# Kernel optimization log

Measured on AMD Instinct MI355X. Metric: run time of the kernel, lower is better.

Reference implementation:

```python
import jax, jax.numpy as jnp
import numpy as np

B, C, H, W = 32, 128, 56, 56
CMAX, OUT, KS, K = 128, 256, 3, 4
HID = 64  # attn_fc hidden width


def setup_inputs() -> dict:
    key = jax.random.key(0)
    ks = jax.random.split(key, 6)
    x = jax.random.normal(ks[0], (B, C, H, W), dtype=jnp.float32)
    weight_bank = jax.random.normal(ks[1], (K, OUT, CMAX, KS, KS), dtype=jnp.float32)
    fc1_w = jax.random.normal(ks[2], (HID, CMAX), dtype=jnp.float32) * (1.0 / np.sqrt(CMAX))
    fc1_b = jnp.zeros((HID,), dtype=jnp.float32)
    fc2_w = jax.random.normal(ks[3], (K, HID), dtype=jnp.float32) * (1.0 / np.sqrt(HID))
    fc2_b = jnp.zeros((K,), dtype=jnp.float32)
    return {"x": x, "weight_bank": weight_bank, "fc1_w": fc1_w, "fc1_b": fc1_b,
            "fc2_w": fc2_w, "fc2_b": fc2_b}


def reference(x, weight_bank, fc1_w, fc1_b, fc2_w, fc2_b):
    b, c, h, w = x.shape
    # AdaptiveAvgPool2d(1) on zero-channel-padded input -> mean over HW, pad channel dim
    pooled = jnp.mean(x, axis=(2, 3))                       # [B, C]
    pooled = jnp.pad(pooled, ((0, 0), (0, CMAX - c)))       # [B, CMAX]
    hdn = jax.nn.relu(pooled @ fc1_w.T + fc1_b)             # [B, 64]
    attn = jax.nn.softmax(hdn @ fc2_w.T + fc2_b, axis=-1)   # [B, K]
    # per-sample kernel synthesis
    weight = jnp.einsum('bk,kocij->bocij', attn, weight_bank[:, :, :c])  # [B,O,C,k,k]
    # single grouped conv instead of B separate conv launches
    lhs = x.reshape(1, b * c, h, w)
    rhs = weight.reshape(b * OUT, c, KS, KS)
    p = KS // 2
    out = jax.lax.conv_general_dilated(
        lhs, rhs, window_strides=(1, 1), padding=[(p, p), (p, p)],
        feature_group_count=b,
        dimension_numbers=('NCHW', 'OIHW', 'NCHW'))
    return out.reshape(b, OUT, h, w)
```

## Files before the change

### kernel.cpp

```cpp
#include <hip/hip_runtime.h>
#include <hip/hip_bf16.h>

#define B_    32
#define C_    128
#define H_    56
#define W_    56
#define OUT_  256
#define K_    4
#define HID_  64
#define HW_   (H_*W_)
#define KV_   (C_*9)
#define PH_   58
#define PW_   58
#define PP_   (PH_*PW_)

typedef __attribute__((ext_vector_type(8))) short short8_t;
typedef __attribute__((ext_vector_type(4))) float float4_t;

typedef __hip_bfloat16 bf16;

__device__ __forceinline__ short f2bf(float v) {
    union { bf16 h; short s; } u; u.h = __float2bfloat16(v); return u.s;
}

typedef __attribute__((address_space(1))) const unsigned int* gas_t;
typedef __attribute__((address_space(3))) unsigned int* las_t;

__device__ __forceinline__ void gl_lds16(const short* g, short* l) {
    __builtin_amdgcn_global_load_lds((gas_t)(const void*)g, (las_t)(void*)l, 16, 0, 0);
}

__global__ __launch_bounds__(256) void dc_xt(const float* __restrict__ x,
                                             short* __restrict__ xTp,
                                             float* __restrict__ pooled) {
    int b = blockIdx.y, n0 = blockIdx.x * 128;
    __shared__ short t[C_][130];
    int lane = threadIdx.x & 63;
    for (int i = threadIdx.x; i < C_*128; i += 256) {
        int c = i >> 7, nn = i & 127;
        int pp = n0 + nn;
        int py = pp / PW_, px = pp - py*PW_;
        bool valid = (pp < PP_) & (py >= 1) & (py <= H_) & (px >= 1) & (px <= W_);
        float v = valid ? x[((size_t)b*C_ + c)*HW_ + (py-1)*W_ + (px-1)] : 0.f;
        t[c][nn] = f2bf(v);
        float s = v;
        for (int off = 32; off > 0; off >>= 1) s += __shfl_down(s, off, 64);
        if (lane == 0 && s != 0.f) atomicAdd(&pooled[b*C_ + c], s);
    }
    __syncthreads();
    for (int i = threadIdx.x; i < 64*128; i += 256) {
        int nn = i >> 6, c2 = (i & 63) * 2;
        int pp = n0 + nn;
        if (pp < PP_) {
            union { unsigned short u[2]; unsigned v; } pk;
            pk.u[0] = (unsigned short)t[c2][nn];
            pk.u[1] = (unsigned short)t[c2+1][nn];
            *(unsigned*)&xTp[((size_t)b*PP_ + pp)*C_ + c2] = pk.v;
        }
    }
}

__global__ __launch_bounds__(64) void dc_attn(const float* __restrict__ pooled,
                                              const float* __restrict__ fc1w,
                                              const float* __restrict__ fc1b,
                                              const float* __restrict__ fc2w,
                                              const float* __restrict__ fc2b,
                                              float* __restrict__ attn) {
    int b = blockIdx.x, h = threadIdx.x;
    __shared__ float pl[C_];
    __shared__ float hdn[HID_];
    __shared__ float logit[K_];
    pl[h]      = pooled[b*C_ + h]      * (1.0f / HW_);
    pl[h + 64] = pooled[b*C_ + 64 + h] * (1.0f / HW_);
    __syncthreads();
    float s = fc1b[h];
    #pragma unroll 8
    for (int c = 0; c < C_; ++c) s += pl[c] * fc1w[h*C_ + c];
    hdn[h] = fmaxf(s, 0.f);
    __syncthreads();
    if (h < K_) {
        float t = fc2b[h];
        #pragma unroll 8
        for (int j = 0; j < HID_; ++j) t += hdn[j] * fc2w[h*HID_ + j];
        logit[h] = t;
    }
    __syncthreads();
    if (h == 0) {
        float m = fmaxf(fmaxf(logit[0], logit[1]), fmaxf(logit[2], logit[3]));
        float e0 = __expf(logit[0]-m), e1 = __expf(logit[1]-m);
        float e2 = __expf(logit[2]-m), e3 = __expf(logit[3]-m);
        float inv = 1.0f / (e0+e1+e2+e3);
        attn[b*K_+0]=e0*inv; attn[b*K_+1]=e1*inv;
        attn[b*K_+2]=e2*inv; attn[b*K_+3]=e3*inv;
    }
}

__global__ __launch_bounds__(256) void dc_wsynth(const float* __restrict__ bank,
                                                 const float* __restrict__ attn,
                                                 bf16* __restrict__ Ws) {
    int o = blockIdx.x;
    int b0 = blockIdx.y * 8;
    __shared__ float wb[4*KV_];
    for (int i = threadIdx.x; i < 4*KV_; i += 256) {
        int kk = i / KV_, r = i - kk*KV_;
        wb[i] = bank[((size_t)kk*OUT_ + o)*KV_ + r];
    }
    __syncthreads();
    for (int bi = 0; bi < 8; ++bi) {
        int b = b0 + bi;
        float a0 = attn[b*K_+0], a1 = attn[b*K_+1];
        float a2 = attn[b*K_+2], a3 = attn[b*K_+3];
        unsigned* dst = (unsigned*)&Ws[((size_t)b*OUT_ + o)*KV_];
        for (int ii = threadIdx.x; ii < KV_/2; ii += 256) {
            int i0 = 2*ii;
            int tap0 = i0 >> 7, c0 = i0 & 127;
            int i1 = i0 + 1;
            int tap1 = i1 >> 7, c1 = i1 & 127;
            float v0 = a0*wb[c0*9+tap0] + a1*wb[KV_+c0*9+tap0]
                     + a2*wb[2*KV_+c0*9+tap0] + a3*wb[3*KV_+c0*9+tap0];
            float v1 = a0*wb[c1*9+tap1] + a1*wb[KV_+c1*9+tap1]
                     + a2*wb[2*KV_+c1*9+tap1] + a3*wb[3*KV_+c1*9+tap1];
            union { unsigned short u[2]; unsigned v; } pk;
            pk.u[0] = (unsigned short)f2bf(v0);
            pk.u[1] = (unsigned short)f2bf(v1);
            dst[ii] = pk.v;
        }
    }
}

__global__ __launch_bounds__(256) void dc_gemm(const short* __restrict__ Ws,
                                               const short* __restrict__ xTp,
                                               float* __restrict__ out) {
    const int b  = blockIdx.z;
    const int m0 = blockIdx.y * 128;
    const int n0 = blockIdx.x * 128;
    const int tid  = threadIdx.x;
    const int lane = tid & 63;
    const int wv   = tid >> 6;
    const int wm   = wv & 1, wn = wv >> 1;
    const int l16  = lane & 15, quad = lane >> 4;

    __shared__ short lA[128*64];
    __shared__ short lB[128*64];

    const short* aG[4];
    const short* bG[4];
    short* aL[4];
    short* bL[4];
    #pragma unroll
    for (int j = 0; j < 4; ++j) {
        int t = 4*wv + j;
        int row = (t >> 1) * 16 + l16;
        int kq  = t & 1;
        aG[j] = Ws + ((size_t)b*OUT_ + m0 + row)*KV_ + kq*32 + quad*8;
        int n = n0 + row;
        int idc = min(n, HW_ - 1);
        int y = idc / W_, xx2 = idc - y * W_;
        int pbc = (y + 1) * PW_ + (xx2 + 1);
        bG[j] = xTp + ((size_t)b*PP_ + pbc)*C_ + kq*32 + quad*8;
        aL[j] = lA + t*512;
        bL[j] = lB + t*512;
    }

    int nidx[4];
    #pragma unroll
    for (int ni = 0; ni < 4; ++ni)
        nidx[ni] = n0 + wn*64 + ni*16 + l16;

    float4_t acc[4][4];
    #pragma unroll
    for (int mi = 0; mi < 4; ++mi)
        #pragma unroll
        for (int ni = 0; ni < 4; ++ni)
            acc[mi][ni] = (float4_t){0.f, 0.f, 0.f, 0.f};

    for (int tap = 0; tap < 9; ++tap) {
        int ty = tap / 3, tx = tap - 3*ty;
        int doff = (ty - 1) * PW_ + (tx - 1);
        #pragma unroll
        for (int half = 0; half < 2; ++half) {
            const int kk = tap*128 + half*64;
            const int cc = half*64;
            #pragma unroll
            for (int j = 0; j < 4; ++j) {
                gl_lds16(aG[j] + kk, aL[j]);
                gl_lds16(bG[j] + doff*C_ + cc, bL[j]);
            }
            __syncthreads();
            #pragma unroll
            for (int kq = 0; kq < 2; ++kq) {
                short8_t af[4], bf[4];
                #pragma unroll
                for (int mi = 0; mi < 4; ++mi)
                    af[mi] = *(const short8_t*)(lA + ((wm*4+mi)*2 + kq)*512 + lane*8);
                #pragma unroll
                for (int ni = 0; ni < 4; ++ni)
                    bf[ni] = *(const short8_t*)(lB + ((wn*4+ni)*2 + kq)*512 + lane*8);
                #pragma unroll
                for (int mi = 0; mi < 4; ++mi)
                    #pragma unroll
                    for (int ni = 0; ni < 4; ++ni)
                        acc[mi][ni] = __builtin_amdgcn_mfma_f32_16x16x32_bf16(
                            af[mi], bf[ni], acc[mi][ni], 0, 0, 0);
            }
            __syncthreads();
        }
    }

    const size_t obase = (size_t)b * OUT_ * HW_;
    #pragma unroll
    for (int mi = 0; mi < 4; ++mi) {
        int m = m0 + wm*64 + mi*16 + quad*4;
        #pragma unroll
        for (int ni = 0; ni < 4; ++ni) {
            int n = nidx[ni];
            if (n < HW_) {
                float* op = out + obase + (size_t)m * HW_ + n;
                #pragma unroll
                for (int r = 0; r < 4; ++r)
                    op[(size_t)r * HW_] = acc[mi][ni][r];
            }
        }
    }
}

extern "C" void kernel_launch(void* const* d_in, const int* in_sizes, int n_in,
                              void* d_out, int out_size, void* d_ws, size_t ws_size,
                              hipStream_t stream) {
    const float* x    = (const float*)d_in[0];
    const float* bank = (const float*)d_in[1];
    const float* fc1w = (const float*)d_in[2];
    const float* fc1b = (const float*)d_in[3];
    const float* fc2w = (const float*)d_in[4];
    const float* fc2b = (const float*)d_in[5];
    float* out = (float*)d_out;

    char* ws = (char*)d_ws;
    float* pooled = (float*)ws;
    float* attn   = (float*)(ws + 16*1024);
    bf16*  Ws     = (bf16*) (ws + 32*1024);
    short* xTp    = (short*)(ws + 32*1024 + 18874368);

    hipMemsetAsync(pooled, 0, B_*C_*sizeof(float), stream);
    dc_xt    <<<dim3(27, B_), 256, 0, stream>>>(x, xTp, pooled);
    dc_attn  <<<B_,     64, 0, stream>>>(pooled, fc1w, fc1b, fc2w, fc2b, attn);
    dc_wsynth<<<dim3(OUT_, 4), 256, 0, stream>>>(bank, attn, Ws);
    dc_gemm  <<<dim3(25, 2, B_), 256, 0, stream>>>((const short*)Ws, xTp, out);
}
```

Before: 357.9 us.

## Double-buffer LDS tiles in conv GEMM and swizzle workgroups across XCDs

The GEMM main loop now double-buffers its LDS tiles. Global-to-LDS loads for the next K stage are issued before computing the current one, and one barrier per stage replaces two, so load latency can overlap MFMA work. The grid is flattened to 1D, and the block index is remapped so consecutive workgroups on each of the 8 XCDs handle adjacent tiles, which should improve L2 reuse. Doubling LDS to 64KB per block may reduce occupancy.

```diff
diff --git a/kernel.cpp b/kernel.cpp
--- a/kernel.cpp
+++ b/kernel.cpp
@@ -131,22 +131,29 @@
 __global__ __launch_bounds__(256) void dc_gemm(const short* __restrict__ Ws,
                                                const short* __restrict__ xTp,
                                                float* __restrict__ out) {
-    const int b  = blockIdx.z;
-    const int m0 = blockIdx.y * 128;
-    const int n0 = blockIdx.x * 128;
+    const int nwg = 25 * 2 * B_;
+    const int cpx = nwg >> 3;
+    int orig = blockIdx.x;
+    int swz  = (orig & 7) * cpx + (orig >> 3);
+    const int bx  = swz % 25;
+    const int byz = swz / 25;
+    const int by  = byz & 1;
+    const int b   = byz >> 1;
+
+    const int m0 = by * 128;
+    const int n0 = bx * 128;
     const int tid  = threadIdx.x;
     const int lane = tid & 63;
     const int wv   = tid >> 6;
     const int wm   = wv & 1, wn = wv >> 1;
     const int l16  = lane & 15, quad = lane >> 4;
 
-    __shared__ short lA[128*64];
-    __shared__ short lB[128*64];
+    __shared__ short lA[2][8192];
+    __shared__ short lB[2][8192];
 
     const short* aG[4];
     const short* bG[4];
-    short* aL[4];
-    short* bL[4];
+    int segOff[4];
     #pragma unroll
     for (int j = 0; j < 4; ++j) {
         int t = 4*wv + j;
@@ -158,8 +165,7 @@
         int y = idc / W_, xx2 = idc - y * W_;
         int pbc = (y + 1) * PW_ + (xx2 + 1);
         bG[j] = xTp + ((size_t)b*PP_ + pbc)*C_ + kq*32 + quad*8;
-        aL[j] = lA + t*512;
-        bL[j] = lB + t*512;
+        segOff[j] = t * 512;
     }
 
     int nidx[4];
@@ -174,37 +180,46 @@
         for (int ni = 0; ni < 4; ++ni)
             acc[mi][ni] = (float4_t){0.f, 0.f, 0.f, 0.f};
 
-    for (int tap = 0; tap < 9; ++tap) {
+    auto stage = [&](int s, int buf) {
+        int tap = s >> 1;
         int ty = tap / 3, tx = tap - 3*ty;
-        int doff = (ty - 1) * PW_ + (tx - 1);
-        #pragma unroll
-        for (int half = 0; half < 2; ++half) {
-            const int kk = tap*128 + half*64;
-            const int cc = half*64;
+        int doff = ((ty - 1) * PW_ + (tx - 1)) * C_;
+        int ka = s * 64;
+        int cb = (s & 1) * 64;
+        #pragma unroll
+        for (int j = 0; j < 4; ++j) {
+            gl_lds16(aG[j] + ka,        lA[buf] + segOff[j]);
+            gl_lds16(bG[j] + doff + cb, lB[buf] + segOff[j]);
+        }
+    };
+
+    auto compute = [&](int buf) {
+        #pragma unroll
+        for (int kq = 0; kq < 2; ++kq) {
+            short8_t af[4], bf[4];
             #pragma unroll
-            for (int j = 0; j < 4; ++j) {
-                gl_lds16(aG[j] + kk, aL[j]);
-                gl_lds16(bG[j] + doff*C_ + cc, bL[j]);
-            }
-            __syncthreads();
+            for (int mi = 0; mi < 4; ++mi)
+                af[mi] = *(const short8_t*)(lA[buf] + ((wm*4+mi)*2 + kq)*512 + lane*8);
             #pragma unroll
-            for (int kq = 0; kq < 2; ++kq) {
-                short8_t af[4], bf[4];
-                #pragma unroll
-                for (int mi = 0; mi < 4; ++mi)
-                    af[mi] = *(const short8_t*)(lA + ((wm*4+mi)*2 + kq)*512 + lane*8);
+            for (int ni = 0; ni < 4; ++ni)
+                bf[ni] = *(const short8_t*)(lB[buf] + ((wn*4+ni)*2 + kq)*512 + lane*8);
+            #pragma unroll
+            for (int mi = 0; mi < 4; ++mi)
                 #pragma unroll
                 for (int ni = 0; ni < 4; ++ni)
-                    bf[ni] = *(const short8_t*)(lB + ((wn*4+ni)*2 + kq)*512 + lane*8);
-                #pragma unroll
-                for (int mi = 0; mi < 4; ++mi)
-                    #pragma unroll
-                    for (int ni = 0; ni < 4; ++ni)
-                        acc[mi][ni] = __builtin_amdgcn_mfma_f32_16x16x32_bf16(
-                            af[mi], bf[ni], acc[mi][ni], 0, 0, 0);
-            }
-            __syncthreads();
-        }
+                    acc[mi][ni] = __builtin_amdgcn_mfma_f32_16x16x32_bf16(
+                        af[mi], bf[ni], acc[mi][ni], 0, 0, 0);
+        }
+    };
+
+    stage(0, 0);
+    __syncthreads();
+    int cur = 0;
+    for (int s = 0; s < 18; ++s) {
+        if (s < 17) stage(s + 1, cur ^ 1);
+        compute(cur);
+        __syncthreads();
+        cur ^= 1;
     }
 
     const size_t obase = (size_t)b * OUT_ * HW_;
@@ -245,5 +260,5 @@
     dc_xt    <<<dim3(27, B_), 256, 0, stream>>>(x, xTp, pooled);
     dc_attn  <<<B_,     64, 0, stream>>>(pooled, fc1w, fc1b, fc2w, fc2b, attn);
     dc_wsynth<<<dim3(OUT_, 4), 256, 0, stream>>>(bank, attn, Ws);
-    dc_gemm  <<<dim3(25, 2, B_), 256, 0, stream>>>((const short*)Ws, xTp, out);
-}
+    dc_gemm  <<<dim3(1600), 256, 0, stream>>>((const short*)Ws, xTp, out);
+}
```

New measurement: 384.7 us. 7.5% more time.
